# Kernel optimization log

Measured on AMD Instinct MI355X. Metric: run time of the kernel, lower is better.

## Reference

```python
import jax, jax.numpy as jnp
import numpy as np

N_NODES = 100000
N_EDGES = 1600000
F_IN = 64
CONVS = [128, 128, 64]
DECODER_HID = 128
N_CLASSES = 2


def _glorot(key, shape):
    fan_in = shape[1]
    lim = 1.0 / np.sqrt(fan_in)
    return jax.random.uniform(key, shape, jnp.float32, -lim, lim)


def setup_inputs() -> dict:
    key = jax.random.key(0)
    ks = jax.random.split(key, 16)
    x = jax.random.normal(ks[0], (N_NODES, F_IN), jnp.float32)
    edge_index = jax.random.randint(ks[1], (2, N_EDGES), 0, N_NODES, jnp.int32)
    dims = [F_IN] + CONVS  # [64,128,128,64]
    inp = {"x": x, "edge_index": edge_index}
    ki = 2
    for i in range(len(CONVS)):
        d_in, d_out = dims[i], dims[i + 1]
        inp[f"Wl{i}"] = _glorot(ks[ki], (d_out, d_in)); ki += 1
        inp[f"bl{i}"] = jnp.zeros((d_out,), jnp.float32)
        inp[f"Wr{i}"] = _glorot(ks[ki], (d_out, d_in)); ki += 1
    inp["Wd1"] = _glorot(ks[ki], (DECODER_HID, CONVS[-1])); ki += 1
    inp["bd1"] = jnp.zeros((DECODER_HID,), jnp.float32)
    inp["Wd2"] = _glorot(ks[ki], (N_CLASSES, DECODER_HID)); ki += 1
    inp["bd2"] = jnp.zeros((N_CLASSES,), jnp.float32)
    return inp


def _sage_conv(x, src, dst, inv_deg, Wl, bl, Wr):
    # gather source features per edge, scatter-mean onto destinations
    msg = x[src]                                          # [E, F]
    agg = jax.ops.segment_sum(msg, dst, num_segments=N_NODES)
    agg = agg * inv_deg[:, None]                          # mean aggregation
    # out = lin_l(mean_neighbors) + lin_r(x_self)
    return agg @ Wl.T + bl + x @ Wr.T


def reference(x, edge_index, Wl0, bl0, Wr0, Wl1, bl1, Wr1, Wl2, bl2, Wr2, Wd1, bd1, Wd2, bd2):
    src = edge_index[0]
    dst = edge_index[1]
    deg = jax.ops.segment_sum(jnp.ones((src.shape[0],), x.dtype), dst, num_segments=N_NODES)
    inv_deg = jnp.where(deg > 0, 1.0 / jnp.maximum(deg, 1.0), 0.0)
    params = [(Wl0, bl0, Wr0), (Wl1, bl1, Wr1), (Wl2, bl2, Wr2)]
    h = x
    for i, (Wl, bl, Wr) in enumerate(params):
        h = _sage_conv(h, src, dst, inv_deg, Wl, bl, Wr)
        if i != len(params) - 1:
            h = jax.nn.relu(h)
    # decoder: ReLU -> Linear(64,128) -> ReLU -> Linear(128,2)
    h = jax.nn.relu(h)
    h = jax.nn.relu(h @ Wd1.T + bd1)
    return h @ Wd2.T + bd2
```

## Files before the change

### kernel.cpp

```cpp
#include <hip/hip_runtime.h>
#include <cstdint>
#include <cstddef>

#define NN 100000
#define NE 1600000
#define BSH 9
#define NBUCK 196
#define CAP 9216
#define P3_CHUNK 8192
#define P3_BLOCKS 196

typedef __attribute__((ext_vector_type(8))) short short8;
typedef __attribute__((ext_vector_type(4))) float f32x4;


__device__ inline unsigned pack_split(float v) {
    unsigned u = __builtin_bit_cast(unsigned, v);
    unsigned hi = (u + 0x7fffu + ((u >> 16) & 1u)) >> 16;
    float vh = __builtin_bit_cast(float, hi << 16);
    float r = v - vh;
    unsigned u2 = __builtin_bit_cast(unsigned, r);
    unsigned lo = (u2 + 0x7fffu + ((u2 >> 16) & 1u)) >> 16;
    return hi | (lo << 16);
}

__device__ inline unsigned short rnb(float v) {
    unsigned u = __builtin_bit_cast(unsigned, v);
    return (unsigned short)((u + 0x7fffu + ((u >> 16) & 1u)) >> 16);
}

__device__ inline float bf2f(unsigned short u) {
    return __builtin_bit_cast(float, (unsigned)u << 16);
}


__global__ __launch_bounds__(256) void k_init_gcur(int* gcur) {
    int t = threadIdx.x;
    if (t < NBUCK) gcur[t] = t * CAP;
}

__global__ __launch_bounds__(256) void k_partition(const int* __restrict__ srce, const int* __restrict__ dste,
                                                   int* __restrict__ gcur, int* __restrict__ tmp) {
    __shared__ int h[NBUCK], lstart[NBUCK], gbase[NBUCK], scn[256];
    __shared__ int s_pack[P3_CHUNK];
    __shared__ int s_gad[P3_CHUNK];
    const int tid = threadIdx.x;
    const int base = blockIdx.x * P3_CHUNK;
    if (tid < NBUCK) h[tid] = 0;
    __syncthreads();
    int rank[P3_CHUNK / 256];
#pragma unroll
    for (int i = 0; i < P3_CHUNK / 256; i++) {
        int idx = base + i * 256 + tid;
        if (idx < NE) rank[i] = atomicAdd(&h[dste[idx] >> BSH], 1);
    }
    __syncthreads();
    int hv = (tid < NBUCK) ? h[tid] : 0;
    if (tid < NBUCK) gbase[tid] = atomicAdd(&gcur[tid], hv);
    scn[tid] = hv;
    __syncthreads();
    for (int off = 1; off < 256; off <<= 1) {
        int u = 0;
        if (tid >= off) u = scn[tid - off];
        __syncthreads();
        scn[tid] += u;
        __syncthreads();
    }
    if (tid < NBUCK) lstart[tid] = scn[tid] - hv;
    __syncthreads();
#pragma unroll
    for (int i = 0; i < P3_CHUNK / 256; i++) {
        int idx = base + i * 256 + tid;
        if (idx < NE) {
            int d = dste[idx], s = srce[idx];
            int b = d >> BSH;
            int slot = lstart[b] + rank[i];
            s_pack[slot] = (s << BSH) | (d & ((1 << BSH) - 1));
            s_gad[slot] = gbase[b] + rank[i];
        }
    }
    __syncthreads();
    int chunkN = NE - base;
    if (chunkN > P3_CHUNK) chunkN = P3_CHUNK;
#pragma unroll
    for (int i = 0; i < P3_CHUNK / 256; i++) {
        int slot = i * 256 + tid;
        if (slot < chunkN) tmp[s_gad[slot]] = s_pack[slot];
    }
}

__global__ __launch_bounds__(256) void k_bucket(const int* __restrict__ tmp, const int* __restrict__ gend,
                                                int* __restrict__ row_ptr, int* __restrict__ rc,
                                                int* __restrict__ col, float* __restrict__ invd) {
    __shared__ int cnt[512], cur[512], scn[256];
    const int b = blockIdx.x, tid = threadIdx.x;
    const int base = b * CAP;
    const int n = gend[b] - base;
    cnt[tid] = 0;
    cnt[tid + 256] = 0;
    __syncthreads();
    for (int k = tid; k < n; k += 256) atomicAdd(&cnt[tmp[base + k] & 511], 1);
    __syncthreads();
    int c0 = cnt[2 * tid], c1 = cnt[2 * tid + 1], s = c0 + c1;
    scn[tid] = s;
    __syncthreads();
    for (int off = 1; off < 256; off <<= 1) {
        int u = 0;
        if (tid >= off) u = scn[tid - off];
        __syncthreads();
        scn[tid] += u;
        __syncthreads();
    }
    int excl = scn[tid] - s;
    int node = (b << BSH) + 2 * tid;
    if (node < NN) {
        row_ptr[node] = base + excl;
        rc[node] = c0;
        invd[node] = c0 ? 1.0f / (float)c0 : 0.0f;
    }
    if (node + 1 < NN) {
        row_ptr[node + 1] = base + excl + c0;
        rc[node + 1] = c1;
        invd[node + 1] = c1 ? 1.0f / (float)c1 : 0.0f;
    }
    cur[2 * tid] = base + excl;
    cur[2 * tid + 1] = base + excl + c0;
    __syncthreads();
    for (int k = tid; k < n; k += 256) {
        int p = tmp[base + k];
        int pos = atomicAdd(&cur[p & 511], 1);
        col[pos] = p >> BSH;
    }
}


__global__ __launch_bounds__(256) void k_xhi(const float* __restrict__ x, unsigned short* __restrict__ Xh) {
    int i = blockIdx.x * 256 + threadIdx.x;
    float4 v = ((const float4*)x)[i];
    ushort4 o = {rnb(v.x), rnb(v.y), rnb(v.z), rnb(v.w)};
    ((ushort4*)Xh)[i] = o;
}

__global__ __launch_bounds__(256) void k_wsplit(const float* __restrict__ Wl0, const float* __restrict__ Wr0,
                                                const float* __restrict__ Wl1, const float* __restrict__ Wr1,
                                                const float* __restrict__ Wl2, const float* __restrict__ Wr2,
                                                const float* __restrict__ Wd1, const float* __restrict__ bl2,
                                                unsigned short* __restrict__ Wh, unsigned short* __restrict__ Wl,
                                                float* __restrict__ biasPQ) {
    int i = blockIdx.x * 256 + threadIdx.x;
    float v = 0.f;
    bool valid = true;
    if (i < 8192) v = Wl0[i];
    else if (i < 16384) v = Wr0[i - 8192];
    else if (i < 32768) v = Wl1[i - 16384];
    else if (i < 49152) v = Wr1[i - 32768];
    else if (i < 57344) v = Wl2[i - 49152];
    else if (i < 65536) v = Wr2[i - 57344];
    else if (i < 73728) v = Wd1[i - 65536];
    else valid = false;
    if (valid) {
        unsigned ps = pack_split(v);
        Wh[i] = (unsigned short)ps;
        Wl[i] = (unsigned short)(ps >> 16);
    }
    if (i >= 73728 && i < 73856) {
        int j = i - 73728;
        biasPQ[j] = (j < 64) ? 0.f : bl2[j - 64];
    }
}


__global__ __launch_bounds__(256) void k_agg64h(const unsigned short* __restrict__ Xh, const int* __restrict__ row_ptr,
                                                const int* __restrict__ rc, const int* __restrict__ col,
                                                const float* __restrict__ invd,
                                                unsigned short* __restrict__ Ah, unsigned short* __restrict__ Al) {
    int node = blockIdx.x * 4 + (threadIdx.x >> 6);
    int lane = threadIdx.x & 63;
    int start = row_ptr[node], end = start + rc[node];
    float a0 = 0.f, a1 = 0.f, a2 = 0.f, a3 = 0.f, a4 = 0.f, a5 = 0.f, a6 = 0.f, a7 = 0.f;
    for (int cs = start; cs < end; cs += 64) {
        int n = end - cs;
        if (n > 64) n = 64;
        int my = (lane < n) ? col[cs + lane] : 0;
        int j = 0;
        for (; j + 8 <= n; j += 8) {
            int s0 = __shfl(my, j + 0), s1 = __shfl(my, j + 1);
            int s2 = __shfl(my, j + 2), s3 = __shfl(my, j + 3);
            int s4 = __shfl(my, j + 4), s5 = __shfl(my, j + 5);
            int s6 = __shfl(my, j + 6), s7 = __shfl(my, j + 7);
            float v0 = bf2f(Xh[(size_t)s0 * 64 + lane]);
            float v1 = bf2f(Xh[(size_t)s1 * 64 + lane]);
            float v2 = bf2f(Xh[(size_t)s2 * 64 + lane]);
            float v3 = bf2f(Xh[(size_t)s3 * 64 + lane]);
            float v4 = bf2f(Xh[(size_t)s4 * 64 + lane]);
            float v5 = bf2f(Xh[(size_t)s5 * 64 + lane]);
            float v6 = bf2f(Xh[(size_t)s6 * 64 + lane]);
            float v7 = bf2f(Xh[(size_t)s7 * 64 + lane]);
            a0 += v0; a1 += v1; a2 += v2; a3 += v3;
            a4 += v4; a5 += v5; a6 += v6; a7 += v7;
        }
        for (; j < n; j++) {
            int s = __shfl(my, j);
            a0 += bf2f(Xh[(size_t)s * 64 + lane]);
        }
    }
    float acc = ((a0 + a1) + (a2 + a3)) + ((a4 + a5) + (a6 + a7));
    unsigned ps = pack_split(acc * invd[node]);
    __builtin_nontemporal_store((unsigned short)ps, Ah + (size_t)node * 64 + lane);
    __builtin_nontemporal_store((unsigned short)(ps >> 16), Al + (size_t)node * 64 + lane);
}

__global__ __launch_bounds__(256) void k_agg128h(const unsigned short* __restrict__ Gh, const int* __restrict__ row_ptr,
                                                 const int* __restrict__ rc, const int* __restrict__ col,
                                                 const float* __restrict__ invd,
                                                 unsigned short* __restrict__ Ah, unsigned short* __restrict__ Al) {
    int node = blockIdx.x * 4 + (threadIdx.x >> 6);
    int lane = threadIdx.x & 63;
    int start = row_ptr[node], end = start + rc[node];
    float ax0 = 0.f, ax1 = 0.f, ax2 = 0.f, ax3 = 0.f, ax4 = 0.f, ax5 = 0.f, ax6 = 0.f, ax7 = 0.f;
    float ay0 = 0.f, ay1 = 0.f, ay2 = 0.f, ay3 = 0.f, ay4 = 0.f, ay5 = 0.f, ay6 = 0.f, ay7 = 0.f;
    for (int cs = start; cs < end; cs += 64) {
        int n = end - cs;
        if (n > 64) n = 64;
        int my = (lane < n) ? col[cs + lane] : 0;
        int j = 0;
        for (; j + 8 <= n; j += 8) {
            int s0 = __shfl(my, j + 0), s1 = __shfl(my, j + 1);
            int s2 = __shfl(my, j + 2), s3 = __shfl(my, j + 3);
            int s4 = __shfl(my, j + 4), s5 = __shfl(my, j + 5);
            int s6 = __shfl(my, j + 6), s7 = __shfl(my, j + 7);
            unsigned u0 = *(const unsigned*)(Gh + (size_t)s0 * 128 + 2 * lane);
            unsigned u1 = *(const unsigned*)(Gh + (size_t)s1 * 128 + 2 * lane);
            unsigned u2 = *(const unsigned*)(Gh + (size_t)s2 * 128 + 2 * lane);
            unsigned u3 = *(const unsigned*)(Gh + (size_t)s3 * 128 + 2 * lane);
            unsigned u4 = *(const unsigned*)(Gh + (size_t)s4 * 128 + 2 * lane);
            unsigned u5 = *(const unsigned*)(Gh + (size_t)s5 * 128 + 2 * lane);
            unsigned u6 = *(const unsigned*)(Gh + (size_t)s6 * 128 + 2 * lane);
            unsigned u7 = *(const unsigned*)(Gh + (size_t)s7 * 128 + 2 * lane);
            ax0 += bf2f((unsigned short)u0); ay0 += bf2f((unsigned short)(u0 >> 16));
            ax1 += bf2f((unsigned short)u1); ay1 += bf2f((unsigned short)(u1 >> 16));
            ax2 += bf2f((unsigned short)u2); ay2 += bf2f((unsigned short)(u2 >> 16));
            ax3 += bf2f((unsigned short)u3); ay3 += bf2f((unsigned short)(u3 >> 16));
            ax4 += bf2f((unsigned short)u4); ay4 += bf2f((unsigned short)(u4 >> 16));
            ax5 += bf2f((unsigned short)u5); ay5 += bf2f((unsigned short)(u5 >> 16));
            ax6 += bf2f((unsigned short)u6); ay6 += bf2f((unsigned short)(u6 >> 16));
            ax7 += bf2f((unsigned short)u7); ay7 += bf2f((unsigned short)(u7 >> 16));
        }
        for (; j < n; j++) {
            int s = __shfl(my, j);
            unsigned u = *(const unsigned*)(Gh + (size_t)s * 128 + 2 * lane);
            ax0 += bf2f((unsigned short)u);
            ay0 += bf2f((unsigned short)(u >> 16));
        }
    }
    float w = invd[node];
    float sx = (((ax0 + ax1) + (ax2 + ax3)) + ((ax4 + ax5) + (ax6 + ax7))) * w;
    float sy = (((ay0 + ay1) + (ay2 + ay3)) + ((ay4 + ay5) + (ay6 + ay7))) * w;
    unsigned px = pack_split(sx), py = pack_split(sy);
    __builtin_nontemporal_store((px & 0xffffu) | (py << 16), (unsigned*)(Ah + (size_t)node * 128 + 2 * lane));
    __builtin_nontemporal_store((px >> 16) | (py & 0xffff0000u), (unsigned*)(Al + (size_t)node * 128 + 2 * lane));
}

__global__ __launch_bounds__(256) void k_aggPh(const unsigned short* __restrict__ Ph, const float* __restrict__ Qf,
                                               const int* __restrict__ row_ptr, const int* __restrict__ rc,
                                               const int* __restrict__ col, const float* __restrict__ invd,
                                               unsigned short* __restrict__ Hh, unsigned short* __restrict__ Hl) {
    int node = blockIdx.x * 4 + (threadIdx.x >> 6);
    int lane = threadIdx.x & 63;
    int start = row_ptr[node], end = start + rc[node];
    float a0 = 0.f, a1 = 0.f, a2 = 0.f, a3 = 0.f, a4 = 0.f, a5 = 0.f, a6 = 0.f, a7 = 0.f;
    for (int cs = start; cs < end; cs += 64) {
        int n = end - cs;
        if (n > 64) n = 64;
        int my = (lane < n) ? col[cs + lane] : 0;
        int j = 0;
        for (; j + 8 <= n; j += 8) {
            int s0 = __shfl(my, j + 0), s1 = __shfl(my, j + 1);
            int s2 = __shfl(my, j + 2), s3 = __shfl(my, j + 3);
            int s4 = __shfl(my, j + 4), s5 = __shfl(my, j + 5);
            int s6 = __shfl(my, j + 6), s7 = __shfl(my, j + 7);
            float v0 = bf2f(Ph[(size_t)s0 * 64 + lane]);
            float v1 = bf2f(Ph[(size_t)s1 * 64 + lane]);
            float v2 = bf2f(Ph[(size_t)s2 * 64 + lane]);
            float v3 = bf2f(Ph[(size_t)s3 * 64 + lane]);
            float v4 = bf2f(Ph[(size_t)s4 * 64 + lane]);
            float v5 = bf2f(Ph[(size_t)s5 * 64 + lane]);
            float v6 = bf2f(Ph[(size_t)s6 * 64 + lane]);
            float v7 = bf2f(Ph[(size_t)s7 * 64 + lane]);
            a0 += v0; a1 += v1; a2 += v2; a3 += v3;
            a4 += v4; a5 += v5; a6 += v6; a7 += v7;
        }
        for (; j < n; j++) {
            int s = __shfl(my, j);
            a0 += bf2f(Ph[(size_t)s * 64 + lane]);
        }
    }
    float acc = ((a0 + a1) + (a2 + a3)) + ((a4 + a5) + (a6 + a7));
    float v = Qf[(size_t)node * 64 + lane] + invd[node] * acc;
    unsigned ps = pack_split(fmaxf(v, 0.f));
    __builtin_nontemporal_store((unsigned short)ps, Hh + (size_t)node * 64 + lane);
    __builtin_nontemporal_store((unsigned short)(ps >> 16), Hl + (size_t)node * 64 + lane);
}


#define LA 40

template <int K, int AFMT>
__device__ inline void mgp(const unsigned short* __restrict__ Ah_g, const unsigned short* __restrict__ Al_g,
                           const float* __restrict__ Af_g,
                           const unsigned short* __restrict__ Wh_g, const unsigned short* __restrict__ Wl_g,
                           int m0, unsigned short* sAh, unsigned short* sAl,
                           unsigned short* sBh, unsigned short* sBl,
                           f32x4 (&acc)[4][4], int tid, int wm, int wn, int l15, int quad) {
    const int srow = tid >> 1, sc = (tid & 1) * 16;
#pragma unroll 1
    for (int kt = 0; kt < K; kt += 32) {
        __syncthreads();
        int gr = m0 + srow;
        uint4 h0 = {0, 0, 0, 0}, h1 = {0, 0, 0, 0}, l0 = {0, 0, 0, 0}, l1 = {0, 0, 0, 0};
        if (AFMT == 0) {
            if (gr < NN) {
                const uint4* ph = (const uint4*)(Ah_g + (size_t)gr * K + kt + sc);
                h0 = ph[0]; h1 = ph[1];
                const uint4* pl = (const uint4*)(Al_g + (size_t)gr * K + kt + sc);
                l0 = pl[0]; l1 = pl[1];
            }
        } else {
            if (gr < NN) {
                const float4* pf = (const float4*)(Af_g + (size_t)gr * K + kt + sc);
                float4 f0 = pf[0], f1 = pf[1], f2 = pf[2], f3 = pf[3];
                float fs[16] = {f0.x, f0.y, f0.z, f0.w, f1.x, f1.y, f1.z, f1.w,
                                f2.x, f2.y, f2.z, f2.w, f3.x, f3.y, f3.z, f3.w};
                alignas(16) unsigned short hh[16], ll[16];
#pragma unroll
                for (int i = 0; i < 16; i++) {
                    unsigned ps = pack_split(fs[i]);
                    hh[i] = (unsigned short)ps;
                    ll[i] = (unsigned short)(ps >> 16);
                }
                h0 = *(const uint4*)&hh[0]; h1 = *(const uint4*)&hh[8];
                l0 = *(const uint4*)&ll[0]; l1 = *(const uint4*)&ll[8];
            }
        }
        const uint4* qh = (const uint4*)(Wh_g + srow * K + kt + sc);
        uint4 b0 = qh[0], b1 = qh[1];
        const uint4* ql = (const uint4*)(Wl_g + srow * K + kt + sc);
        uint4 b2 = ql[0], b3 = ql[1];
        *(uint4*)(sAh + srow * LA + sc) = h0; *(uint4*)(sAh + srow * LA + sc + 8) = h1;
        *(uint4*)(sAl + srow * LA + sc) = l0; *(uint4*)(sAl + srow * LA + sc + 8) = l1;
        *(uint4*)(sBh + srow * LA + sc) = b0; *(uint4*)(sBh + srow * LA + sc + 8) = b1;
        *(uint4*)(sBl + srow * LA + sc) = b2; *(uint4*)(sBl + srow * LA + sc + 8) = b3;
        __syncthreads();
        short8 ah[4], al[4], bh[4], bl[4];
#pragma unroll
        for (int t = 0; t < 4; t++) {
            ah[t] = *(const short8*)(sAh + (wm + t * 16 + l15) * LA + quad * 8);
            al[t] = *(const short8*)(sAl + (wm + t * 16 + l15) * LA + quad * 8);
            bh[t] = *(const short8*)(sBh + (wn + t * 16 + l15) * LA + quad * 8);
            bl[t] = *(const short8*)(sBl + (wn + t * 16 + l15) * LA + quad * 8);
        }
#pragma unroll
        for (int mt = 0; mt < 4; mt++)
#pragma unroll
            for (int nt = 0; nt < 4; nt++) {
                acc[mt][nt] = __builtin_amdgcn_mfma_f32_16x16x32_bf16(ah[mt], bh[nt], acc[mt][nt], 0, 0, 0);
                acc[mt][nt] = __builtin_amdgcn_mfma_f32_16x16x32_bf16(ah[mt], bl[nt], acc[mt][nt], 0, 0, 0);
                acc[mt][nt] = __builtin_amdgcn_mfma_f32_16x16x32_bf16(al[mt], bh[nt], acc[mt][nt], 0, 0, 0);
            }
    }
}

template <int K1, int K2, int AF1, int AF2, bool RELU, int OMODE>
__global__ __launch_bounds__(256) void k_mgemm(
    const unsigned short* A1h, const unsigned short* A1l, const float* A1f,
    const unsigned short* A2h, const unsigned short* A2l, const float* A2f,
    const unsigned short* __restrict__ W1h, const unsigned short* __restrict__ W1l,
    const unsigned short* __restrict__ W2h, const unsigned short* __restrict__ W2l,
    const float* __restrict__ bias, float* Cf, unsigned short* Chi, unsigned short* Clo,
    unsigned short* Ph, float* Qf,
    const float* __restrict__ Wd2, const float* __restrict__ bd2, float* outp) {
    __shared__ unsigned short sAh[128 * LA], sAl[128 * LA], sBh[128 * LA], sBl[128 * LA];
    const int tid = threadIdx.x;
    const int m0 = blockIdx.x * 128;
    const int wave = tid >> 6, lane = tid & 63;
    const int wm = (wave & 1) * 64, wn = (wave >> 1) * 64;
    const int l15 = lane & 15, quad = lane >> 4;
    f32x4 acc[4][4];
#pragma unroll
    for (int i = 0; i < 4; i++)
#pragma unroll
        for (int j = 0; j < 4; j++) acc[i][j] = (f32x4){0.f, 0.f, 0.f, 0.f};

    mgp<K1, AF1>(A1h, A1l, A1f, W1h, W1l, m0, sAh, sAl, sBh, sBl, acc, tid, wm, wn, l15, quad);
    if (K2 > 0) mgp<K2, AF2>(A2h, A2l, A2f, W2h, W2l, m0, sAh, sAl, sBh, sBl, acc, tid, wm, wn, l15, quad);

    if (OMODE == 3) {
        __syncthreads();
        float* sOut = (float*)sAh;
        sOut[tid] = 0.f;
        __syncthreads();
        float w0[4], w1[4], bv[4];
#pragma unroll
        for (int nt = 0; nt < 4; nt++) {
            int cg = wn + nt * 16 + l15;
            w0[nt] = Wd2[cg];
            w1[nt] = Wd2[128 + cg];
            bv[nt] = bias[cg];
        }
#pragma unroll
        for (int mt = 0; mt < 4; mt++) {
#pragma unroll
            for (int r = 0; r < 4; r++) {
                float s0 = 0.f, s1 = 0.f;
#pragma unroll
                for (int nt = 0; nt < 4; nt++) {
                    float v = fmaxf(acc[mt][nt][r] + bv[nt], 0.f);
                    s0 += v * w0[nt];
                    s1 += v * w1[nt];
                }
                s0 += __shfl_xor(s0, 1); s1 += __shfl_xor(s1, 1);
                s0 += __shfl_xor(s0, 2); s1 += __shfl_xor(s1, 2);
                s0 += __shfl_xor(s0, 4); s1 += __shfl_xor(s1, 4);
                s0 += __shfl_xor(s0, 8); s1 += __shfl_xor(s1, 8);
                if (l15 == 0) {
                    int lr = wm + mt * 16 + quad * 4 + r;
                    atomicAdd(&sOut[lr * 2 + 0], s0);
                    atomicAdd(&sOut[lr * 2 + 1], s1);
                }
            }
        }
        __syncthreads();
        int lr = tid >> 1, c = tid & 1;
        int row = m0 + lr;
        if (row < NN) outp[(size_t)row * 2 + c] = sOut[lr * 2 + c] + bd2[c];
        return;
    }

#pragma unroll
    for (int mt = 0; mt < 4; mt++) {
        int rbase = m0 + wm + mt * 16 + quad * 4;
#pragma unroll
        for (int nt = 0; nt < 4; nt++) {
            int cg = wn + nt * 16 + l15;
            float bv = bias[cg];
#pragma unroll
            for (int r = 0; r < 4; r++) {
                int row = rbase + r;
                if (row < NN) {
                    float v = acc[mt][nt][r] + bv;
                    if (RELU) v = fmaxf(v, 0.f);
                    if (OMODE == 0) {
                        Cf[(size_t)row * 128 + cg] = v;
                    } else if (OMODE == 1) {
                        unsigned ps = pack_split(v);
                        Chi[(size_t)row * 128 + cg] = (unsigned short)ps;
                        Clo[(size_t)row * 128 + cg] = (unsigned short)(ps >> 16);
                    } else {
                        if (cg < 64) Ph[(size_t)row * 64 + cg] = rnb(v);
                        else Qf[(size_t)row * 64 + cg - 64] = v;
                    }
                }
            }
        }
    }
}


extern "C" void kernel_launch(void* const* d_in, const int* in_sizes, int n_in,
                              void* d_out, int out_size, void* d_ws, size_t ws_size,
                              hipStream_t stream) {
    const float* x   = (const float*)d_in[0];
    const int*   ei  = (const int*)d_in[1];
    const float* Wl0 = (const float*)d_in[2];
    const float* bl0 = (const float*)d_in[3];
    const float* Wr0 = (const float*)d_in[4];
    const float* Wl1 = (const float*)d_in[5];
    const float* bl1 = (const float*)d_in[6];
    const float* Wr1 = (const float*)d_in[7];
    const float* Wl2 = (const float*)d_in[8];
    const float* bl2 = (const float*)d_in[9];
    const float* Wr2 = (const float*)d_in[10];
    const float* Wd1 = (const float*)d_in[11];
    const float* bd1 = (const float*)d_in[12];
    const float* Wd2 = (const float*)d_in[13];
    const float* bd2 = (const float*)d_in[14];
    float* out = (float*)d_out;

    char* ws = (char*)d_ws;
    size_t off = 0;
    auto alloc = [&](size_t bytes) {
        char* p = ws + off;
        off = (off + bytes + 255) & ~(size_t)255;
        return p;
    };
    int*            gcur    = (int*)alloc((size_t)NBUCK * 4);
    int*            row_ptr = (int*)alloc((size_t)NN * 4);
    int*            rc      = (int*)alloc((size_t)NN * 4);
    float*          invd    = (float*)alloc((size_t)NN * 4);
    float*          biasPQ  = (float*)alloc(128 * 4);
    unsigned short* Wh      = (unsigned short*)alloc((size_t)73728 * 2);
    unsigned short* Wl      = (unsigned short*)alloc((size_t)73728 * 2);
    int*            col     = (int*)alloc((size_t)NBUCK * CAP * 4);
    char*           R1      = alloc((size_t)NN * 128 * 4);
    char*           R2      = alloc((size_t)NN * 128 * 4);
    (void)ws_size;

    int*            tmp   = (int*)R1;
    unsigned short* Xh    = (unsigned short*)R1;
    unsigned short* Agg0h = (unsigned short*)(R1 + 12800000);
    unsigned short* Agg0l = (unsigned short*)(R1 + 25600000);
    unsigned short* Agg1h = (unsigned short*)R1;
    unsigned short* Agg1l = (unsigned short*)(R1 + 25600000);
    unsigned short* Ph    = (unsigned short*)R1;
    float*          Qf    = (float*)(R1 + 12800000);
    unsigned short* G0h   = (unsigned short*)R2;
    unsigned short* G0l   = (unsigned short*)(R2 + 25600000);
    unsigned short* H1h   = G0h;
    unsigned short* H1l   = G0l;
    unsigned short* h2h   = (unsigned short*)R2;
    unsigned short* h2l   = (unsigned short*)(R2 + 12800000);

    const unsigned short* WL0h = Wh,         * WL0l = Wl;
    const unsigned short* WR0h = Wh + 8192,  * WR0l = Wl + 8192;
    const unsigned short* WL1h = Wh + 16384, * WL1l = Wl + 16384;
    const unsigned short* WR1h = Wh + 32768, * WR1l = Wl + 32768;
    const unsigned short* WPQh = Wh + 49152, * WPQl = Wl + 49152;
    const unsigned short* WD1h = Wh + 65536, * WD1l = Wl + 65536;

    const int* srce = ei;
    const int* dste = ei + NE;

    k_init_gcur<<<1, 256, 0, stream>>>(gcur);
    k_partition<<<P3_BLOCKS, 256, 0, stream>>>(srce, dste, gcur, tmp);
    k_bucket<<<NBUCK, 256, 0, stream>>>(tmp, gcur, row_ptr, rc, col, invd);

    k_wsplit<<<289, 256, 0, stream>>>(Wl0, Wr0, Wl1, Wr1, Wl2, Wr2, Wd1, bl2, Wh, Wl, biasPQ);
    k_xhi<<<(NN * 64 / 4 + 255) / 256, 256, 0, stream>>>(x, Xh);

    const int gGemm = (NN + 127) / 128;
    const int gNode = NN / 4;

    k_agg64h<<<gNode, 256, 0, stream>>>(Xh, row_ptr, rc, col, invd, Agg0h, Agg0l);
    k_mgemm<64, 64, 0, 1, true, 1><<<gGemm, 256, 0, stream>>>(
        Agg0h, Agg0l, nullptr, nullptr, nullptr, x,
        WL0h, WL0l, WR0h, WR0l, bl0, nullptr, G0h, G0l, nullptr, nullptr,
        nullptr, nullptr, nullptr);

    k_agg128h<<<gNode, 256, 0, stream>>>(G0h, row_ptr, rc, col, invd, Agg1h, Agg1l);
    k_mgemm<128, 128, 0, 0, true, 1><<<gGemm, 256, 0, stream>>>(
        Agg1h, Agg1l, nullptr, G0h, G0l, nullptr,
        WL1h, WL1l, WR1h, WR1l, bl1, nullptr, H1h, H1l, nullptr, nullptr,
        nullptr, nullptr, nullptr);

    k_mgemm<128, 0, 0, 0, false, 2><<<gGemm, 256, 0, stream>>>(
        H1h, H1l, nullptr, nullptr, nullptr, nullptr,
        WPQh, WPQl, nullptr, nullptr, biasPQ, nullptr, nullptr, nullptr, Ph, Qf,
        nullptr, nullptr, nullptr);
    k_aggPh<<<gNode, 256, 0, stream>>>(Ph, Qf, row_ptr, rc, col, invd, h2h, h2l);

    k_mgemm<64, 0, 0, 0, true, 3><<<gGemm, 256, 0, stream>>>(
        h2h, h2l, nullptr, nullptr, nullptr, nullptr,
        WD1h, WD1l, nullptr, nullptr, bd1, nullptr, nullptr, nullptr, nullptr, nullptr,
        Wd2, bd2, out);
}
```

Baseline: 467.0 us.

## Merge setup kernels, halve partition chunk, and prefetch next GEMM K-tile into registers

Folds the gcur init, weight split and x-to-bf16 conversion into one launch, which cuts kernel launch count. The partition kernel now uses 4096-edge chunks over 391 blocks, and its tmp buffer moves to R2 so it does not clash with Xh in R1. The GEMM main loop now loads the next K-tile's global data into registers while MFMAs run on the current tile. This is software pipelining that hides load latency, at the cost of extra registers that may reduce occupancy.

```diff
diff --git a/kernel.cpp b/kernel.cpp
--- a/kernel.cpp
+++ b/kernel.cpp
@@ -7,8 +7,8 @@
 #define BSH 9
 #define NBUCK 196
 #define CAP 9216
-#define P3_CHUNK 8192
-#define P3_BLOCKS 196
+#define P3_CHUNK 4096
+#define P3_BLOCKS 391
 
 typedef __attribute__((ext_vector_type(8))) short short8;
 typedef __attribute__((ext_vector_type(4))) float f32x4;
@@ -33,11 +33,6 @@
     return __builtin_bit_cast(float, (unsigned)u << 16);
 }
 
-
-__global__ __launch_bounds__(256) void k_init_gcur(int* gcur) {
-    int t = threadIdx.x;
-    if (t < NBUCK) gcur[t] = t * CAP;
-}
 
 __global__ __launch_bounds__(256) void k_partition(const int* __restrict__ srce, const int* __restrict__ dste,
                                                    int* __restrict__ gcur, int* __restrict__ tmp) {
@@ -134,20 +129,24 @@
 }
 
 
-__global__ __launch_bounds__(256) void k_xhi(const float* __restrict__ x, unsigned short* __restrict__ Xh) {
-    int i = blockIdx.x * 256 + threadIdx.x;
-    float4 v = ((const float4*)x)[i];
-    ushort4 o = {rnb(v.x), rnb(v.y), rnb(v.z), rnb(v.w)};
-    ((ushort4*)Xh)[i] = o;
-}
-
-__global__ __launch_bounds__(256) void k_wsplit(const float* __restrict__ Wl0, const float* __restrict__ Wr0,
-                                                const float* __restrict__ Wl1, const float* __restrict__ Wr1,
-                                                const float* __restrict__ Wl2, const float* __restrict__ Wr2,
-                                                const float* __restrict__ Wd1, const float* __restrict__ bl2,
-                                                unsigned short* __restrict__ Wh, unsigned short* __restrict__ Wl,
-                                                float* __restrict__ biasPQ) {
-    int i = blockIdx.x * 256 + threadIdx.x;
+#define XHI_BLOCKS 6250
+
+__global__ __launch_bounds__(256) void k_conv(const float* __restrict__ x,
+                                              const float* __restrict__ Wl0, const float* __restrict__ Wr0,
+                                              const float* __restrict__ Wl1, const float* __restrict__ Wr1,
+                                              const float* __restrict__ Wl2, const float* __restrict__ Wr2,
+                                              const float* __restrict__ Wd1, const float* __restrict__ bl2,
+                                              unsigned short* __restrict__ Xh,
+                                              unsigned short* __restrict__ Wh, unsigned short* __restrict__ Wl,
+                                              float* __restrict__ biasPQ, int* __restrict__ gcur) {
+    if (blockIdx.x < XHI_BLOCKS) {
+        int i = blockIdx.x * 256 + threadIdx.x;
+        float4 v = ((const float4*)x)[i];
+        ushort4 o = {rnb(v.x), rnb(v.y), rnb(v.z), rnb(v.w)};
+        ((ushort4*)Xh)[i] = o;
+        return;
+    }
+    int i = (blockIdx.x - XHI_BLOCKS) * 256 + threadIdx.x;
     float v = 0.f;
     bool valid = true;
     if (i < 8192) v = Wl0[i];
@@ -166,6 +165,10 @@
     if (i >= 73728 && i < 73856) {
         int j = i - 73728;
         biasPQ[j] = (j < 64) ? 0.f : bl2[j - 64];
+    }
+    if (i >= 73856 && i < 73856 + NBUCK) {
+        int j = i - 73856;
+        gcur[j] = j * CAP;
     }
 }
 
@@ -306,6 +309,42 @@
 #define LA 40
 
 template <int K, int AFMT>
+__device__ inline void mg_load(const unsigned short* __restrict__ Ah_g, const unsigned short* __restrict__ Al_g,
+                               const float* __restrict__ Af_g,
+                               const unsigned short* __restrict__ Wh_g, const unsigned short* __restrict__ Wl_g,
+                               int gr, int srow, int sc, int kt, uint4* r) {
+    r[0] = r[1] = r[2] = r[3] = (uint4){0, 0, 0, 0};
+    if (AFMT == 0) {
+        if (gr < NN) {
+            const uint4* ph = (const uint4*)(Ah_g + (size_t)gr * K + kt + sc);
+            r[0] = ph[0]; r[1] = ph[1];
+            const uint4* pl = (const uint4*)(Al_g + (size_t)gr * K + kt + sc);
+            r[2] = pl[0]; r[3] = pl[1];
+        }
+    } else {
+        if (gr < NN) {
+            const float4* pf = (const float4*)(Af_g + (size_t)gr * K + kt + sc);
+            float4 f0 = pf[0], f1 = pf[1], f2 = pf[2], f3 = pf[3];
+            float fs[16] = {f0.x, f0.y, f0.z, f0.w, f1.x, f1.y, f1.z, f1.w,
+                            f2.x, f2.y, f2.z, f2.w, f3.x, f3.y, f3.z, f3.w};
+            alignas(16) unsigned short hh[16], ll[16];
+#pragma unroll
+            for (int i = 0; i < 16; i++) {
+                unsigned ps = pack_split(fs[i]);
+                hh[i] = (unsigned short)ps;
+                ll[i] = (unsigned short)(ps >> 16);
+            }
+            r[0] = *(const uint4*)&hh[0]; r[1] = *(const uint4*)&hh[8];
+            r[2] = *(const uint4*)&ll[0]; r[3] = *(const uint4*)&ll[8];
+        }
+    }
+    const uint4* qh = (const uint4*)(Wh_g + srow * K + kt + sc);
+    r[4] = qh[0]; r[5] = qh[1];
+    const uint4* ql = (const uint4*)(Wl_g + srow * K + kt + sc);
+    r[6] = ql[0]; r[7] = ql[1];
+}
+
+template <int K, int AFMT>
 __device__ inline void mgp(const unsigned short* __restrict__ Ah_g, const unsigned short* __restrict__ Al_g,
                            const float* __restrict__ Af_g,
                            const unsigned short* __restrict__ Wh_g, const unsigned short* __restrict__ Wl_g,
@@ -313,44 +352,19 @@
                            unsigned short* sBh, unsigned short* sBl,
                            f32x4 (&acc)[4][4], int tid, int wm, int wn, int l15, int quad) {
     const int srow = tid >> 1, sc = (tid & 1) * 16;
+    const int gr = m0 + srow;
+    uint4 cur[8];
+    mg_load<K, AFMT>(Ah_g, Al_g, Af_g, Wh_g, Wl_g, gr, srow, sc, 0, cur);
 #pragma unroll 1
     for (int kt = 0; kt < K; kt += 32) {
         __syncthreads();
-        int gr = m0 + srow;
-        uint4 h0 = {0, 0, 0, 0}, h1 = {0, 0, 0, 0}, l0 = {0, 0, 0, 0}, l1 = {0, 0, 0, 0};
-        if (AFMT == 0) {
-            if (gr < NN) {
-                const uint4* ph = (const uint4*)(Ah_g + (size_t)gr * K + kt + sc);
-                h0 = ph[0]; h1 = ph[1];
-                const uint4* pl = (const uint4*)(Al_g + (size_t)gr * K + kt + sc);
-                l0 = pl[0]; l1 = pl[1];
-            }
-        } else {
-            if (gr < NN) {
-                const float4* pf = (const float4*)(Af_g + (size_t)gr * K + kt + sc);
-                float4 f0 = pf[0], f1 = pf[1], f2 = pf[2], f3 = pf[3];
-                float fs[16] = {f0.x, f0.y, f0.z, f0.w, f1.x, f1.y, f1.z, f1.w,
-                                f2.x, f2.y, f2.z, f2.w, f3.x, f3.y, f3.z, f3.w};
-                alignas(16) unsigned short hh[16], ll[16];
-#pragma unroll
-                for (int i = 0; i < 16; i++) {
-                    unsigned ps = pack_split(fs[i]);
-                    hh[i] = (unsigned short)ps;
-                    ll[i] = (unsigned short)(ps >> 16);
-                }
-                h0 = *(const uint4*)&hh[0]; h1 = *(const uint4*)&hh[8];
-                l0 = *(const uint4*)&ll[0]; l1 = *(const uint4*)&ll[8];
-            }
-        }
-        const uint4* qh = (const uint4*)(Wh_g + srow * K + kt + sc);
-        uint4 b0 = qh[0], b1 = qh[1];
-        const uint4* ql = (const uint4*)(Wl_g + srow * K + kt + sc);
-        uint4 b2 = ql[0], b3 = ql[1];
-        *(uint4*)(sAh + srow * LA + sc) = h0; *(uint4*)(sAh + srow * LA + sc + 8) = h1;
-        *(uint4*)(sAl + srow * LA + sc) = l0; *(uint4*)(sAl + srow * LA + sc + 8) = l1;
-        *(uint4*)(sBh + srow * LA + sc) = b0; *(uint4*)(sBh + srow * LA + sc + 8) = b1;
-        *(uint4*)(sBl + srow * LA + sc) = b2; *(uint4*)(sBl + srow * LA + sc + 8) = b3;
-        __syncthreads();
+        *(uint4*)(sAh + srow * LA + sc) = cur[0]; *(uint4*)(sAh + srow * LA + sc + 8) = cur[1];
+        *(uint4*)(sAl + srow * LA + sc) = cur[2]; *(uint4*)(sAl + srow * LA + sc + 8) = cur[3];
+        *(uint4*)(sBh + srow * LA + sc) = cur[4]; *(uint4*)(sBh + srow * LA + sc + 8) = cur[5];
+        *(uint4*)(sBl + srow * LA + sc) = cur[6]; *(uint4*)(sBl + srow * LA + sc + 8) = cur[7];
+        __syncthreads();
+        if (kt + 32 < K)
+            mg_load<K, AFMT>(Ah_g, Al_g, Af_g, Wh_g, Wl_g, gr, srow, sc, kt + 32, cur);
         short8 ah[4], al[4], bh[4], bl[4];
 #pragma unroll
         for (int t = 0; t < 4; t++) {
@@ -505,7 +519,6 @@
     char*           R2      = alloc((size_t)NN * 128 * 4);
     (void)ws_size;
 
-    int*            tmp   = (int*)R1;
     unsigned short* Xh    = (unsigned short*)R1;
     unsigned short* Agg0h = (unsigned short*)(R1 + 12800000);
     unsigned short* Agg0l = (unsigned short*)(R1 + 25600000);
@@ -513,6 +526,7 @@
     unsigned short* Agg1l = (unsigned short*)(R1 + 25600000);
     unsigned short* Ph    = (unsigned short*)R1;
     float*          Qf    = (float*)(R1 + 12800000);
+    int*            tmp   = (int*)R2;
     unsigned short* G0h   = (unsigned short*)R2;
     unsigned short* G0l   = (unsigned short*)(R2 + 25600000);
     unsigned short* H1h   = G0h;
@@ -530,12 +544,11 @@
     const int* srce = ei;
     const int* dste = ei + NE;
 
-    k_init_gcur<<<1, 256, 0, stream>>>(gcur);
+    k_conv<<<XHI_BLOCKS + 290, 256, 0, stream>>>(x, Wl0, Wr0, Wl1, Wr1, Wl2, Wr2, Wd1, bl2,
+                                                 Xh, Wh, Wl, biasPQ, gcur);
+
     k_partition<<<P3_BLOCKS, 256, 0, stream>>>(srce, dste, gcur, tmp);
     k_bucket<<<NBUCK, 256, 0, stream>>>(tmp, gcur, row_ptr, rc, col, invd);
-
-    k_wsplit<<<289, 256, 0, stream>>>(Wl0, Wr0, Wl1, Wr1, Wl2, Wr2, Wd1, bl2, Wh, Wl, biasPQ);
-    k_xhi<<<(NN * 64 / 4 + 255) / 256, 256, 0, stream>>>(x, Xh);
 
     const int gGemm = (NN + 127) / 128;
     const int gNode = NN / 4;
```

New measurement: 465.0 us. Within noise of the previous version (-0.4%).
